# Kernel optimization log

Hardware: AMD Instinct MI355X
Metric: run time of the kernel (lower is better)

Reference implementation:

```python
import jax, jax.numpy as jnp
import numpy as np
from jax.scipy.special import logsumexp

B, N, D = 8, 1500, 256
ITERS = 50


def _mlp(x, W1, b1, W2, b2, W3, b3):
    # DETR-style MLP: ReLU between layers, linear last
    h = jax.nn.relu(x @ W1 + b1)
    h = jax.nn.relu(h @ W2 + b2)
    return h @ W3 + b3


def _log_sinkhorn(Z, log_mu, log_nu, iters):
    # Z: [b, m+1, n+1]; loop-carried dual potentials u, v
    u0 = jnp.zeros_like(log_mu)
    v0 = jnp.zeros_like(log_nu)

    def step(carry, _):
        u, v = carry
        u = log_mu - logsumexp(Z + v[:, None, :], axis=2)
        v = log_nu - logsumexp(Z + u[:, :, None], axis=1)
        return (u, v), None

    (u, v), _ = jax.lax.scan(step, (u0, v0), None, length=iters)
    return Z + u[:, :, None] + v[:, None, :]


def _log_optimal_transport(scores, alpha, iters):
    b, m, n = scores.shape
    bins0 = jnp.broadcast_to(alpha, (b, m, 1))
    bins1 = jnp.broadcast_to(alpha, (b, 1, n))
    a = jnp.broadcast_to(alpha, (b, 1, 1))
    couplings = jnp.concatenate(
        [jnp.concatenate([scores, bins0], -1), jnp.concatenate([bins1, a], -1)], 1
    )  # [b, m+1, n+1]
    dt = scores.dtype
    norm = -jnp.log(jnp.asarray(m + n, dt))
    log_mu = jnp.concatenate([jnp.full((m,), norm, dt), jnp.log(jnp.asarray(n, dt))[None] + norm])
    log_nu = jnp.concatenate([jnp.full((n,), norm, dt), jnp.log(jnp.asarray(m, dt))[None] + norm])
    log_mu = jnp.broadcast_to(log_mu[None], (b, m + 1))
    log_nu = jnp.broadcast_to(log_nu[None], (b, n + 1))
    Z = _log_sinkhorn(couplings, log_mu, log_nu, iters)
    return Z - norm


def setup_inputs() -> dict:
    key = jax.random.key(0)
    k = jax.random.split(key, 6)
    s = 0.05
    return {
        "quer_feat": jax.random.normal(k[0], (B, N, D), jnp.float32),
        "pos_start": jax.random.normal(k[1], (B, N, D), jnp.float32),
        "pos_end": jax.random.normal(k[2], (B, N, D), jnp.float32),
        "W1": jax.random.normal(k[3], (2 * D, D), jnp.float32) * s,
        "b1": jnp.zeros((D,), jnp.float32),
        "W2": jax.random.normal(k[4], (D, D), jnp.float32) * s,
        "b2": jnp.zeros((D,), jnp.float32),
        "W3": jax.random.normal(k[5], (D, D), jnp.float32) * s,
        "b3": jnp.zeros((D,), jnp.float32),
        "bin_score": jnp.asarray(1.0, jnp.float32),
        "iters": ITERS,
    }


def reference(quer_feat, pos_start, pos_end, W1, b1, W2, b2, W3, b3, bin_score, iters):
    # forward_single with shared_projection + similarity_based + sinkhorn
    f1 = _mlp(jnp.concatenate([quer_feat, pos_end], -1), W1, b1, W2, b2, W3, b3)
    f2 = _mlp(jnp.concatenate([quer_feat, pos_start], -1), W1, b1, W2, b2, W3, b3)
    scores = jnp.einsum("bnc,bmc->bnm", f1, f2) / jnp.sqrt(jnp.asarray(D, f1.dtype))
    i = jnp.arange(scores.shape[1])
    scores = scores.at[:, i, i].set(-jnp.inf)  # no self-connection
    Z = _log_optimal_transport(scores, bin_score, iters)
    return jnp.exp(Z)
```

## Files before the change

kernel.cpp:

```cpp
#include <hip/hip_runtime.h>
#include <hip/hip_fp16.h>

#define BATCH 8
#define NPTS 1500
#define DIM 256
#define M1 1501
#define KH 1536
#define MROWS 24000
#define ITERS 50
#define MU_PT (1.0f / 3000.0f)
#define MU_BIN 0.5f

typedef _Float16 half8 __attribute__((ext_vector_type(8)));
typedef float f32x4 __attribute__((ext_vector_type(4)));

__device__ __forceinline__ float4 ld4(const float* p){ return *(const float4*)p; }

__global__ void prep_w_kernel(const float* __restrict__ W1, const float* __restrict__ W2,
                              const float* __restrict__ W3, __half* __restrict__ Wt1,
                              __half* __restrict__ Wt2, __half* __restrict__ Wt3)
{
  int gid = blockIdx.x * 256 + threadIdx.x;
  if (gid < 512 * 256) {
    int n = gid >> 9, k = gid & 511;
    Wt1[gid] = __float2half(W1[k * 256 + n]);
  } else if (gid < 512 * 256 + 256 * 256) {
    int g = gid - 512 * 256; int n = g >> 8, k = g & 255;
    Wt2[g] = __float2half(W2[k * 256 + n]);
  } else if (gid < 512 * 256 + 2 * 256 * 256) {
    int g = gid - 512 * 256 - 256 * 256; int n = g >> 8, k = g & 255;
    Wt3[g] = __float2half(W3[k * 256 + n]);
  }
}

template<int MODE>
__global__ __launch_bounds__(256) void mfma_gemm_kernel(
    const float* __restrict__ Aq, const float* __restrict__ Ap_end,
    const float* __restrict__ Ap_start, const __half* __restrict__ Ah,
    const __half* __restrict__ Bh, const float* __restrict__ bias,
    __half* __restrict__ out)
{
  const int K = (MODE == 0) ? 512 : 256;
  const int M = (MODE == 3) ? NPTS : MROWS;
  __shared__ _Float16 As[128][40];
  __shared__ _Float16 Bs[128][40];
  const int t = threadIdx.x;
  const int lane = t & 63;
  const int wave = t >> 6;
  const int quad = lane >> 4, l15 = lane & 15;
  const int wm = wave & 1, wn = wave >> 1;
  const int m0 = blockIdx.x * 128;
  const int n0 = blockIdx.y * 128;
  const int b  = (MODE == 3) ? blockIdx.z : 0;
  const __half* F1 = Ah + (size_t)b * NPTS * 256;
  const __half* F2 = Ah + (size_t)(12000 + b * NPTS) * 256;

  f32x4 acc[4][4];
#pragma unroll
  for (int i = 0; i < 4; ++i)
#pragma unroll
    for (int j = 0; j < 4; ++j) acc[i][j] = (f32x4){0.f, 0.f, 0.f, 0.f};

  const int sr = t >> 1;
  const int c0 = (t & 1) * 16;

  for (int kt = 0; kt < K; kt += 32) {
    {
      int grow = m0 + sr;
      if (MODE == 0) {
        union { half8 v[2]; _Float16 s[16]; } U;
        if (grow < M) {
          int col = kt + c0;
          int r12 = (grow < 12000) ? grow : grow - 12000;
          const float* src;
          if (col < 256) src = Aq + (size_t)r12 * 256 + col;
          else src = ((grow < 12000) ? Ap_end : Ap_start) + (size_t)r12 * 256 + (col - 256);
#pragma unroll
          for (int i = 0; i < 4; ++i) {
            float4 w = ld4(src + 4 * i);
            U.s[4*i+0] = (_Float16)w.x; U.s[4*i+1] = (_Float16)w.y;
            U.s[4*i+2] = (_Float16)w.z; U.s[4*i+3] = (_Float16)w.w;
          }
        } else {
#pragma unroll
          for (int i = 0; i < 16; ++i) U.s[i] = (_Float16)0.f;
        }
        *(half8*)&As[sr][c0]     = U.v[0];
        *(half8*)&As[sr][c0 + 8] = U.v[1];
      } else {
        const __half* src = ((MODE == 3) ? F1 : Ah) + (size_t)grow * 256 + kt + c0;
        uint4 u0 = make_uint4(0,0,0,0), u1 = make_uint4(0,0,0,0);
        if (grow < M) { u0 = *(const uint4*)src; u1 = *(const uint4*)(src + 8); }
        *(uint4*)&As[sr][c0]     = u0;
        *(uint4*)&As[sr][c0 + 8] = u1;
      }
    }
    {
      int n = n0 + sr;
      uint4 u0 = make_uint4(0,0,0,0), u1 = make_uint4(0,0,0,0);
      if (MODE == 3) {
        if (n < NPTS) {
          const __half* src = F2 + (size_t)n * 256 + kt + c0;
          u0 = *(const uint4*)src; u1 = *(const uint4*)(src + 8);
        }
      } else {
        const __half* src = Bh + (size_t)n * K + kt + c0;
        u0 = *(const uint4*)src; u1 = *(const uint4*)(src + 8);
      }
      *(uint4*)&Bs[sr][c0]     = u0;
      *(uint4*)&Bs[sr][c0 + 8] = u1;
    }
    __syncthreads();
    half8 af[4], bf[4];
#pragma unroll
    for (int sm = 0; sm < 4; ++sm)
      af[sm] = *(half8*)&As[wm * 64 + sm * 16 + l15][quad * 8];
#pragma unroll
    for (int sn = 0; sn < 4; ++sn)
      bf[sn] = *(half8*)&Bs[wn * 64 + sn * 16 + l15][quad * 8];
#pragma unroll
    for (int sm = 0; sm < 4; ++sm)
#pragma unroll
      for (int sn = 0; sn < 4; ++sn)
        acc[sm][sn] = __builtin_amdgcn_mfma_f32_16x16x32_f16(af[sm], bf[sn], acc[sm][sn], 0, 0, 0);
    __syncthreads();
  }

  if (MODE == 3) {
    __half* Kb = out + (size_t)b * M1 * KH;
#pragma unroll
    for (int sm = 0; sm < 4; ++sm) {
      int rbase = m0 + wm * 64 + sm * 16 + quad * 4;
#pragma unroll
      for (int reg = 0; reg < 4; ++reg) {
        int gi = rbase + reg;
        if (gi < NPTS) {
#pragma unroll
          for (int sn = 0; sn < 4; ++sn) {
            int gj = n0 + wn * 64 + sn * 16 + l15;
            float v = acc[sm][sn][reg] * 0.0625f;
            float kv = (gj < NPTS && gj != gi) ? __expf(v) : 0.f;
            Kb[(size_t)gi * KH + gj] = __float2half(kv);
          }
        }
      }
    }
  } else {
    float bv[4];
#pragma unroll
    for (int sn = 0; sn < 4; ++sn) bv[sn] = bias[n0 + wn * 64 + sn * 16 + l15];
#pragma unroll
    for (int sm = 0; sm < 4; ++sm) {
      int rbase = m0 + wm * 64 + sm * 16 + quad * 4;
#pragma unroll
      for (int reg = 0; reg < 4; ++reg) {
        int gr = rbase + reg;
        if (gr < MROWS) {
#pragma unroll
          for (int sn = 0; sn < 4; ++sn) {
            int col = n0 + wn * 64 + sn * 16 + l15;
            float v = acc[sm][sn][reg] + bv[sn];
            if (MODE != 2) v = fmaxf(v, 0.f);
            out[(size_t)gr * 256 + col] = __float2half(v);
          }
        }
      }
    }
  }
}

__global__ void bins_kernel(__half* __restrict__ Kh, const float* __restrict__ palpha,
                            float* __restrict__ csum0)
{
  int gid = blockIdx.x * 256 + threadIdx.x;
  if (gid >= BATCH * KH) return;
  int b = gid / KH, x = gid % KH;
  __half He = __float2half(expf(palpha[0]));
  __half* Kb = Kh + (size_t)b * M1 * KH;
  csum0[gid] = 0.f;
  if (x < M1) {
    Kb[(size_t)NPTS * KH + x] = He;
    Kb[(size_t)x * KH + NPTS] = He;
  } else {
    Kb[(size_t)NPTS * KH + x] = __float2half(0.f);
  }
}

__global__ __launch_bounds__(256) void sink_iter_kernel(
    const __half* __restrict__ Kh,
    const float* __restrict__ csum_prev,
    float* __restrict__ csum_cur,
    float* __restrict__ csum_zero,
    float* __restrict__ eu, int first)
{
  const int t = threadIdx.x;
  const int wave = t >> 6, lane = t & 63;
  const int bb = blockIdx.x & 7;
  const int rb = blockIdx.x >> 3;
  const int wv = (rb << 2) | wave;
  const __half* Kb = Kh + (size_t)bb * M1 * KH;
  float* eub = eu + bb * KH;

  __shared__ __align__(16) float wpart[4][KH];

  if (rb == 0) {
    for (int j = t; j < KH; j += 256) csum_zero[bb * KH + j] = 0.f;
  }

  float ev[24];
  if (first) {
#pragma unroll
    for (int k = 0; k < 3; ++k) {
      int cbase = (lane << 3) + (k << 9);
#pragma unroll
      for (int j = 0; j < 8; ++j) ev[k * 8 + j] = (cbase + j < M1) ? 1.0f : 0.f;
    }
  } else {
    const float* cp = csum_prev + bb * KH;
#pragma unroll
    for (int k = 0; k < 3; ++k) {
      int cbase = (lane << 3) + (k << 9);
      float4 a  = *(const float4*)(cp + cbase);
      float4 bq = *(const float4*)(cp + cbase + 4);
      float cs[8] = {a.x, a.y, a.z, a.w, bq.x, bq.y, bq.z, bq.w};
#pragma unroll
      for (int j = 0; j < 8; ++j) {
        int col = cbase + j;
        float nu = (col < NPTS) ? MU_PT : ((col == NPTS) ? MU_BIN : 0.f);
        ev[k * 8 + j] = (col < M1) ? (nu / cs[j]) : 0.f;
      }
    }
  }

  float acc[24];
#pragma unroll
  for (int k = 0; k < 24; ++k) acc[k] = 0.f;

  for (int i = wv; i < M1; i += 256) {
    const __half* row = Kb + (size_t)i * KH;
    float r[24];
    float dot = 0.f;
#pragma unroll
    for (int k = 0; k < 3; ++k) {
      int c = lane + (k << 6);
      union { uint4 u; __half2 h[4]; } U;
      U.u = *(const uint4*)(row + (c << 3));
#pragma unroll
      for (int m = 0; m < 4; ++m) {
        float2 f = __half22float2(U.h[m]);
        r[k * 8 + 2 * m]     = f.x;
        r[k * 8 + 2 * m + 1] = f.y;
      }
      dot += r[k*8+0]*ev[k*8+0] + r[k*8+1]*ev[k*8+1] + r[k*8+2]*ev[k*8+2] + r[k*8+3]*ev[k*8+3]
           + r[k*8+4]*ev[k*8+4] + r[k*8+5]*ev[k*8+5] + r[k*8+6]*ev[k*8+6] + r[k*8+7]*ev[k*8+7];
    }
#pragma unroll
    for (int off = 32; off > 0; off >>= 1) dot += __shfl_xor(dot, off);
    float mu = (i < NPTS) ? MU_PT : MU_BIN;
    float euv = mu / dot;
    if (lane == 0) eub[i] = euv;
#pragma unroll
    for (int k = 0; k < 24; ++k) acc[k] += r[k] * euv;
  }

#pragma unroll
  for (int k = 0; k < 3; ++k) {
    int c = lane + (k << 6);
    float4 a0 = make_float4(acc[k*8+0], acc[k*8+1], acc[k*8+2], acc[k*8+3]);
    float4 a1 = make_float4(acc[k*8+4], acc[k*8+5], acc[k*8+6], acc[k*8+7]);
    *(float4*)&wpart[wave][(c << 3)]     = a0;
    *(float4*)&wpart[wave][(c << 3) + 4] = a1;
  }
  __syncthreads();
  for (int j = t; j < M1; j += 256) {
    float s = wpart[0][j] + wpart[1][j] + wpart[2][j] + wpart[3][j];
    atomicAdd(&csum_cur[bb * KH + j], s);
  }
}

__global__ void final_ev_kernel(const float* __restrict__ csum,
                                float* __restrict__ ev)
{
  int j = blockIdx.x * 256 + threadIdx.x;
  int bb = blockIdx.y;
  if (j >= M1) return;
  float nu = (j < NPTS) ? MU_PT : MU_BIN;
  ev[bb * KH + j] = nu / csum[bb * KH + j];
}

__global__ __launch_bounds__(192) void finalize_kernel(
    const __half* __restrict__ Kh, const float* __restrict__ eu,
    const float* __restrict__ ev, float* __restrict__ out)
{
  int rowid = blockIdx.x;
  int b = rowid / M1, i = rowid % M1;
  const __half* krow = Kh + ((size_t)b * M1 + i) * KH;
  const float* evb = ev + b * KH;
  float* orow = out + (size_t)rowid * M1;
  float scale = eu[b * KH + i] * 3000.0f;
  int c0 = threadIdx.x * 8;
  if (c0 < M1) {
    union { uint4 u; __half2 h[4]; } U;
    U.u = *(const uint4*)(krow + c0);
    float4 e0 = *(const float4*)(evb + c0);
    float4 e1 = *(const float4*)(evb + c0 + 4);
    float f[8], e[8] = {e0.x, e0.y, e0.z, e0.w, e1.x, e1.y, e1.z, e1.w};
#pragma unroll
    for (int m = 0; m < 4; ++m) {
      float2 g = __half22float2(U.h[m]);
      f[2 * m] = g.x; f[2 * m + 1] = g.y;
    }
#pragma unroll
    for (int j = 0; j < 8; ++j) {
      int c = c0 + j;
      if (c < M1) orow[c] = f[j] * e[j] * scale;
    }
  }
}

extern "C" void kernel_launch(void* const* d_in, const int* in_sizes, int n_in,
                              void* d_out, int out_size, void* d_ws, size_t ws_size,
                              hipStream_t stream)
{
  const float* quer      = (const float*)d_in[0];
  const float* pos_start = (const float*)d_in[1];
  const float* pos_end   = (const float*)d_in[2];
  const float* W1 = (const float*)d_in[3];
  const float* b1 = (const float*)d_in[4];
  const float* W2 = (const float*)d_in[5];
  const float* b2 = (const float*)d_in[6];
  const float* W3 = (const float*)d_in[7];
  const float* b3 = (const float*)d_in[8];
  const float* alpha = (const float*)d_in[9];

  char* ws = (char*)d_ws;
  size_t off = 0;
  auto carve = [&](size_t bytes) -> void* {
    void* p = ws + off;
    off += (bytes + 1023) & ~(size_t)1023;
    return p;
  };
  __half* Ha  = (__half*)carve((size_t)MROWS * 256 * 2);
  __half* Hb  = (__half*)carve((size_t)MROWS * 256 * 2);
  __half* Kh  = (__half*)carve((size_t)BATCH * M1 * KH * 2);
  __half* Wt1 = (__half*)carve((size_t)256 * 512 * 2);
  __half* Wt2 = (__half*)carve((size_t)256 * 256 * 2);
  __half* Wt3 = (__half*)carve((size_t)256 * 256 * 2);
  float* csum[3];
  for (int c = 0; c < 3; ++c) csum[c] = (float*)carve((size_t)BATCH * KH * 4);
  float* eu = (float*)carve((size_t)BATCH * KH * 4);
  float* ev = (float*)carve((size_t)BATCH * KH * 4);
  (void)ws_size; (void)in_sizes; (void)n_in; (void)out_size;

  dim3 blk(256);
  prep_w_kernel<<<dim3(1024), blk, 0, stream>>>(W1, W2, W3, Wt1, Wt2, Wt3);
  mfma_gemm_kernel<0><<<dim3(188, 2), blk, 0, stream>>>(quer, pos_end, pos_start, nullptr, Wt1, b1, Ha);
  mfma_gemm_kernel<1><<<dim3(188, 2), blk, 0, stream>>>(nullptr, nullptr, nullptr, Ha, Wt2, b2, Hb);
  mfma_gemm_kernel<2><<<dim3(188, 2), blk, 0, stream>>>(nullptr, nullptr, nullptr, Hb, Wt3, b3, Ha);
  mfma_gemm_kernel<3><<<dim3(12, 12, 8), blk, 0, stream>>>(nullptr, nullptr, nullptr, Ha, nullptr, nullptr, Kh);
  bins_kernel<<<dim3((BATCH * KH + 255) / 256), blk, 0, stream>>>(Kh, alpha, csum[0]);
  for (int it = 0; it < ITERS; ++it) {
    float* prev = csum[(it + 2) % 3];
    float* cur  = csum[it % 3];
    float* znxt = csum[(it + 1) % 3];
    sink_iter_kernel<<<dim3(512), blk, 0, stream>>>(Kh, prev, cur, znxt, eu, it == 0 ? 1 : 0);
  }
  final_ev_kernel<<<dim3(6, 8), blk, 0, stream>>>(csum[(ITERS - 1) % 3], ev);
  finalize_kernel<<<dim3(BATCH * M1), dim3(192), 0, stream>>>(Kh, eu, ev, (float*)d_out);
}
```

Before: 772.3 us.

## Widen sinkhorn blocks to 8 waves with LDS atomics, coalesce finalize rows

The Sinkhorn iteration kernel moves from 4 to 8 waves per block, so each block covers twice as many rows and the row stride doubles. The per-wave shared partial arrays are replaced by a single shared column buffer filled with LDS atomics, then flushed to global memory with global atomics. The finalize kernel now processes one row per wave using coalesced scalar accesses instead of one row per 192-thread block with vector loads. Possible costs are LDS atomic contention, higher register pressure at 512 threads per block, and losing the 128-bit vector loads in finalize.

```diff
diff --git a/kernel.cpp b/kernel.cpp
--- a/kernel.cpp
+++ b/kernel.cpp
@@ -186,7 +186,7 @@
   }
 }
 
-__global__ __launch_bounds__(256) void sink_iter_kernel(
+__global__ __launch_bounds__(512) void sink_iter_kernel(
     const __half* __restrict__ Kh,
     const float* __restrict__ csum_prev,
     float* __restrict__ csum_cur,
@@ -197,15 +197,16 @@
   const int wave = t >> 6, lane = t & 63;
   const int bb = blockIdx.x & 7;
   const int rb = blockIdx.x >> 3;
-  const int wv = (rb << 2) | wave;
+  const int wv = (rb << 3) | wave;
   const __half* Kb = Kh + (size_t)bb * M1 * KH;
   float* eub = eu + bb * KH;
 
-  __shared__ __align__(16) float wpart[4][KH];
+  __shared__ __align__(16) float cpart[KH];
 
   if (rb == 0) {
-    for (int j = t; j < KH; j += 256) csum_zero[bb * KH + j] = 0.f;
-  }
+    for (int j = t; j < KH; j += 512) csum_zero[bb * KH + j] = 0.f;
+  }
+  for (int j = t; j < KH; j += 512) cpart[j] = 0.f;
 
   float ev[24];
   if (first) {
@@ -231,12 +232,13 @@
       }
     }
   }
+  __syncthreads();
 
   float acc[24];
 #pragma unroll
   for (int k = 0; k < 24; ++k) acc[k] = 0.f;
 
-  for (int i = wv; i < M1; i += 256) {
+  for (int i = wv; i < M1; i += 512) {
     const __half* row = Kb + (size_t)i * KH;
     float r[24];
     float dot = 0.f;
@@ -264,17 +266,22 @@
   }
 
 #pragma unroll
-  for (int k = 0; k < 3; ++k) {
-    int c = lane + (k << 6);
-    float4 a0 = make_float4(acc[k*8+0], acc[k*8+1], acc[k*8+2], acc[k*8+3]);
-    float4 a1 = make_float4(acc[k*8+4], acc[k*8+5], acc[k*8+6], acc[k*8+7]);
-    *(float4*)&wpart[wave][(c << 3)]     = a0;
-    *(float4*)&wpart[wave][(c << 3) + 4] = a1;
-  }
+  for (int k = 0; k < 3; ++k)
+#pragma unroll
+    for (int j = 0; j < 8; ++j)
+      atomicAdd(&cpart[(((k << 3) + j) << 6) + lane], acc[k * 8 + j]);
   __syncthreads();
-  for (int j = t; j < M1; j += 256) {
-    float s = wpart[0][j] + wpart[1][j] + wpart[2][j] + wpart[3][j];
-    atomicAdd(&csum_cur[bb * KH + j], s);
+
+  {
+    float* cc = csum_cur + bb * KH;
+#pragma unroll
+    for (int p = 0; p < 3; ++p) {
+      int c = t + (p << 9);
+      int kk = c >> 9, rem = c & 511;
+      int idx = (((kk << 3) + (rem & 7)) << 6) + (rem >> 3);
+      float v = cpart[idx];
+      if (c < M1) atomicAdd(&cc[c], v);
+    }
   }
 }
 
@@ -288,33 +295,23 @@
   ev[bb * KH + j] = nu / csum[bb * KH + j];
 }
 
-__global__ __launch_bounds__(192) void finalize_kernel(
+__global__ __launch_bounds__(256) void finalize_kernel(
     const __half* __restrict__ Kh, const float* __restrict__ eu,
     const float* __restrict__ ev, float* __restrict__ out)
 {
-  int rowid = blockIdx.x;
+  int rowid = blockIdx.x * 4 + (threadIdx.x >> 6);
+  if (rowid >= BATCH * M1) return;
+  int lane = threadIdx.x & 63;
   int b = rowid / M1, i = rowid % M1;
   const __half* krow = Kh + ((size_t)b * M1 + i) * KH;
   const float* evb = ev + b * KH;
   float* orow = out + (size_t)rowid * M1;
   float scale = eu[b * KH + i] * 3000.0f;
-  int c0 = threadIdx.x * 8;
-  if (c0 < M1) {
-    union { uint4 u; __half2 h[4]; } U;
-    U.u = *(const uint4*)(krow + c0);
-    float4 e0 = *(const float4*)(evb + c0);
-    float4 e1 = *(const float4*)(evb + c0 + 4);
-    float f[8], e[8] = {e0.x, e0.y, e0.z, e0.w, e1.x, e1.y, e1.z, e1.w};
-#pragma unroll
-    for (int m = 0; m < 4; ++m) {
-      float2 g = __half22float2(U.h[m]);
-      f[2 * m] = g.x; f[2 * m + 1] = g.y;
-    }
-#pragma unroll
-    for (int j = 0; j < 8; ++j) {
-      int c = c0 + j;
-      if (c < M1) orow[c] = f[j] * e[j] * scale;
-    }
+#pragma unroll
+  for (int k = 0; k < 24; ++k) {
+    int c = lane + (k << 6);
+    if (c < M1)
+      orow[c] = __half2float(krow[c]) * evb[c] * scale;
   }
 }
 
@@ -363,8 +360,8 @@
     float* prev = csum[(it + 2) % 3];
     float* cur  = csum[it % 3];
     float* znxt = csum[(it + 1) % 3];
-    sink_iter_kernel<<<dim3(512), blk, 0, stream>>>(Kh, prev, cur, znxt, eu, it == 0 ? 1 : 0);
+    sink_iter_kernel<<<dim3(512), dim3(512), 0, stream>>>(Kh, prev, cur, znxt, eu, it == 0 ? 1 : 0);
   }
   final_ev_kernel<<<dim3(6, 8), blk, 0, stream>>>(csum[(ITERS - 1) % 3], ev);
-  finalize_kernel<<<dim3(BATCH * M1), dim3(192), 0, stream>>>(Kh, eu, ev, (float*)d_out);
-}
+  finalize_kernel<<<dim3((BATCH * M1 + 3) / 4), blk, 0, stream>>>(Kh, eu, ev, (float*)d_out);
+}
```

Result: slower. 2.161 ms (+179.9%).
